# Performance work log

Measured on AMD Instinct MI355X. Metric: run time of the kernel, lower is better.

## Reference

```python
import jax, jax.numpy as jnp
import numpy as np

DN = ('NHWC', 'HWIO', 'NHWC')
EPS = 1e-3  # Keras BatchNormalization default epsilon


def conv2d(x, w):
    return jax.lax.conv_general_dilated(x, w, (1, 1), 'SAME', dimension_numbers=DN)


def hard_sigmoid(x):
    # Keras ConvLSTM2D default recurrent_activation
    return jnp.clip(0.2 * x + 0.5, 0.0, 1.0)


def convlstm2d(x, Wx, Wh, b):
    """Keras ConvLSTM2D, return_sequences=True. x: (B,T,H,W,C).
    Wx: (3,3,C,4F) input kernel, Wh: (3,3,F,4F) recurrent kernel, b: (4F,).
    Gate order (Keras): i, f, c, o."""
    B, T, H, W, C = x.shape
    F = Wh.shape[2]
    # input-to-gate convs for all timesteps in one batched conv
    xg = conv2d(x.reshape(B * T, H, W, C), Wx) + b          # (B*T,H,W,4F)
    xg = xg.reshape(B, T, H, W, 4 * F).transpose(1, 0, 2, 3, 4)  # (T,B,H,W,4F)

    def step(carry, xg_t):
        h, c = carry
        g = xg_t + conv2d(h, Wh)                            # (B,H,W,4F)
        i, f, cc, o = jnp.split(g, 4, axis=-1)
        i = hard_sigmoid(i)
        f = hard_sigmoid(f)
        o = hard_sigmoid(o)
        c = f * c + i * jnp.tanh(cc)
        h = o * jnp.tanh(c)
        return (h, c), h

    h0 = jnp.zeros((B, H, W, F), x.dtype)
    (_, _), hs = jax.lax.scan(step, (h0, h0), xg)           # hs: (T,B,H,W,F)
    return hs.transpose(1, 0, 2, 3, 4)


def batchnorm(x, gamma, beta):
    # training-mode BN over all axes except channel (last)
    mu = x.mean(axis=(0, 1, 2, 3), keepdims=True)
    var = x.var(axis=(0, 1, 2, 3), keepdims=True)
    return gamma * (x - mu) * jax.lax.rsqrt(var + EPS) + beta


def setup_inputs() -> dict:
    key = jax.random.key(0)
    B, T, H, W, C = 4, 8, 16, 16, 256
    F = 256
    ks = jax.random.split(key, 10)
    s = 0.02
    inp = {
        'input_tensor': jax.random.normal(ks[0], (B, T, H, W, C), jnp.float32),
        'Wx1': jax.random.normal(ks[1], (3, 3, C, 4 * F), jnp.float32) * s,
        'Wh1': jax.random.normal(ks[2], (3, 3, F, 4 * F), jnp.float32) * s,
        'b1': jnp.zeros((4 * F,), jnp.float32),
        'g1': jnp.ones((F,), jnp.float32),
        'be1': jnp.zeros((F,), jnp.float32),
        'Wx2': jax.random.normal(ks[3], (3, 3, F, 4 * F), jnp.float32) * s,
        'Wh2': jax.random.normal(ks[4], (3, 3, F, 4 * F), jnp.float32) * s,
        'b2': jnp.zeros((4 * F,), jnp.float32),
        'g2': jnp.ones((F,), jnp.float32),
        'be2': jnp.zeros((F,), jnp.float32),
        'Wx3': jax.random.normal(ks[5], (3, 3, F, 4 * F), jnp.float32) * s,
        'Wh3': jax.random.normal(ks[6], (3, 3, F, 4 * F), jnp.float32) * s,
        'b3': jnp.zeros((4 * F,), jnp.float32),
        'g3': jnp.ones((F,), jnp.float32),
        'be3': jnp.zeros((F,), jnp.float32),
    }
    return inp


def reference(input_tensor, Wx1, Wh1, b1, g1, be1,
              Wx2, Wh2, b2, g2, be2,
              Wx3, Wh3, b3, g3, be3):
    x = batchnorm(convlstm2d(input_tensor, Wx1, Wh1, b1), g1, be1)
    x = batchnorm(convlstm2d(x, Wx2, Wh2, b2), g2, be2)
    x = batchnorm(convlstm2d(x, Wx3, Wh3, b3), g3, be3)
    return x
```

## Files before the change

### kernel.cpp

```cpp
#include <hip/hip_runtime.h>

#define HW      256
#define COUT    1024
#define TSTEPS  8
#define BN_EPS  1e-3f
#define KTOT    2304

typedef unsigned short u16;
typedef unsigned int   u32;
typedef __attribute__((ext_vector_type(8))) _Float16 v8h;
typedef __attribute__((ext_vector_type(4))) float v4f;

__device__ __forceinline__ u16 f2h(float x) {
    _Float16 h = (_Float16)x; return *(u16*)&h;
}
__device__ __forceinline__ float h2f(u16 u) {
    _Float16 h = *(_Float16*)&u; return (float)h;
}
__device__ __forceinline__ float hsig(float x) {
    return fminf(fmaxf(0.2f * x + 0.5f, 0.f), 1.f);
}

typedef __attribute__((address_space(1))) const unsigned int gas_u32;
typedef __attribute__((address_space(3))) unsigned int las_u32;
__device__ __forceinline__ void gl16(const void* g, void* l) {
    __builtin_amdgcn_global_load_lds((gas_u32*)g, (las_u32*)l, 16, 0, 0);
}

__global__ __launch_bounds__(256, 2) void conv_big_k(
    const u16* __restrict__ apad,
    const u16* __restrict__ wT,
    const float* __restrict__ bias,
    u16* __restrict__ out)
{
    constexpr int KQ = 36;
    __shared__ u16 lds[2 * 16384];

    const int bid = blockIdx.x;
    const int xcd = bid & 7, idx = bid >> 3;
    const int by = (xcd >> 1) * 2 + (idx & 1);
    const int bx = (xcd & 1) * 32 + (idx >> 1);
    const int m0 = bx * 128, n0 = by * 128;
    const int tid = threadIdx.x, lane = tid & 63, w = tid >> 6;
    const int wr = w >> 1, wc = w & 1;
    const int lr = lane >> 3;
    const int g  = (lane & 7) ^ lr;
    const int fr = lane & 15, kc = lane >> 4;

    const char* a_src[4];
    #pragma unroll
    for (int i = 0; i < 4; ++i) {
        int m = m0 + w * 32 + i * 8 + lr;
        int img = m >> 8, pix = m & 255, yy = pix >> 4, xx = pix & 15;
        a_src[i] = (const char*)apad + ((((long)img * 18 + yy) * 18 + xx) * 256 + g * 8) * 2;
    }
    const char* b_src[4];
    #pragma unroll
    for (int i = 0; i < 4; ++i) {
        int n = n0 + w * 32 + i * 8 + lr;
        b_src[i] = (const char*)wT + ((long)n * KTOT + g * 8) * 2;
    }

    int aro[4][2], bro[4][2];
    #pragma unroll
    for (int mi = 0; mi < 4; ++mi) {
        int rl = wr * 64 + mi * 16 + fr;
        #pragma unroll
        for (int ks = 0; ks < 2; ++ks)
            aro[mi][ks] = rl * 128 + ((((ks << 2) | kc) ^ (fr & 7)) << 4);
    }
    #pragma unroll
    for (int ni = 0; ni < 4; ++ni) {
        int nr = wc * 64 + ni * 16 + fr;
        #pragma unroll
        for (int ks = 0; ks < 2; ++ks)
            bro[ni][ks] = 16384 + nr * 128 + ((((ks << 2) | kc) ^ (fr & 7)) << 4);
    }

    v4f acc[4][4];
    #pragma unroll
    for (int mi = 0; mi < 4; ++mi)
        #pragma unroll
        for (int ni = 0; ni < 4; ++ni) acc[mi][ni] = (v4f)0.f;

#define STAGE_B(J) { int j_ = (J); int dxy = j_ >> 2, c64 = j_ & 3;           \
    int dy = (dxy * 11) >> 5; int dx = dxy - dy * 3;                          \
    int aoff = ((dy * 18 + dx) * 256 + c64 * 64) * 2; int boff = j_ * 128;    \
    char* base = (char*)lds + (j_ & 1) * 32768;                               \
    _Pragma("unroll") for (int i = 0; i < 4; ++i)                             \
        gl16(a_src[i] + aoff, base + (w * 32 + i * 8) * 128);                 \
    _Pragma("unroll") for (int i = 0; i < 4; ++i)                             \
        gl16(b_src[i] + boff, base + 16384 + (w * 32 + i * 8) * 128); }

#define COMPUTE_B(J) { const char* base = (const char*)lds + ((J) & 1) * 32768; \
    v8h af[4][2], bf[4][2];                                                   \
    _Pragma("unroll") for (int mi = 0; mi < 4; ++mi)                          \
        _Pragma("unroll") for (int ks = 0; ks < 2; ++ks)                      \
            af[mi][ks] = *(const v8h*)(base + aro[mi][ks]);                   \
    _Pragma("unroll") for (int ni = 0; ni < 4; ++ni)                          \
        _Pragma("unroll") for (int ks = 0; ks < 2; ++ks)                      \
            bf[ni][ks] = *(const v8h*)(base + bro[ni][ks]);                   \
    __builtin_amdgcn_s_setprio(1);                                            \
    _Pragma("unroll") for (int ks = 0; ks < 2; ++ks)                          \
    _Pragma("unroll") for (int mi = 0; mi < 4; ++mi)                          \
    _Pragma("unroll") for (int ni = 0; ni < 4; ++ni)                          \
        acc[mi][ni] = __builtin_amdgcn_mfma_f32_16x16x32_f16(af[mi][ks], bf[ni][ks], acc[mi][ni], 0, 0, 0); \
    __builtin_amdgcn_s_setprio(0); }

    STAGE_B(0);
    for (int kq = 0; kq < KQ; ++kq) {
        int jj = kq + 1 < KQ ? kq + 1 : KQ - 1;
        __builtin_amdgcn_s_barrier();
        STAGE_B(jj);
        asm volatile("s_waitcnt vmcnt(8)" ::: "memory");
        __builtin_amdgcn_s_barrier();
        __builtin_amdgcn_sched_barrier(0);
        COMPUTE_B(kq);
    }
#undef STAGE_B
#undef COMPUTE_B

    #pragma unroll
    for (int mi = 0; mi < 4; ++mi) {
        #pragma unroll
        for (int ni = 0; ni < 4; ++ni) {
            int mrow = m0 + wr * 64 + mi * 16 + ((lane >> 4) << 2);
            int ncol = n0 + wc * 64 + ni * 16 + fr;
            float b0 = bias[(ncol & 3) * 256 + (ncol >> 2)];
            #pragma unroll
            for (int r = 0; r < 4; ++r)
                out[(long)(mrow + r) * COUT + ncol] = f2h(acc[mi][ni][r] + b0);
        }
    }
}

__global__ __launch_bounds__(256, 2) void rec_fused_k(
    const u16* __restrict__ ph_in,
    const u16* __restrict__ wTf,
    const u16* __restrict__ xg,
    float* __restrict__ cbuf,
    float* __restrict__ hs,
    u16* __restrict__ ph_out,
    int t)
{
    __shared__ u16 lds[3 * 2048];

    const int bid = blockIdx.x;
    const int by = (bid & 7) * 2 + ((bid >> 3) & 1);
    const int bx = bid >> 4;
    const int m0 = bx * 32, n0 = by * 64;
    const int tid = threadIdx.x, lane = tid & 63, w = tid >> 6;
    const int wr = w >> 1, wc = w & 1;
    const int fr = lane & 15, kc = lane >> 4;

    const char* a_src;
    {
        int rt = tid >> 3;
        int gg = (lane & 7) ^ (rt & 7);
        int m = m0 + rt;
        int img = m >> 8, pix = m & 255, yy = pix >> 4, xx = pix & 15;
        a_src = (const char*)ph_in + ((((long)img * 18 + yy) * 18 + xx) * 256 + gg * 8) * 2;
    }
    const char* b_base0 = (const char*)wTf + ((long)(by * 4 + wc * 2 + 0) * 72) * 1024 + lane * 16;
    const char* b_base1 = (const char*)wTf + ((long)(by * 4 + wc * 2 + 1) * 72) * 1024 + lane * 16;

    int aro[2];
    #pragma unroll
    for (int ks = 0; ks < 2; ++ks)
        aro[ks] = (wr * 16 + fr) * 128 + ((((ks << 2) | kc) ^ (fr & 7)) << 4);

    v4f acc0 = (v4f)0.f, acc1 = (v4f)0.f;

#define STAGE_A(J) { int j_ = (J); int dxy = j_ >> 2, c64 = j_ & 3;           \
    int dy = (dxy * 11) >> 5; int dx = dxy - dy * 3;                          \
    int aoff = ((dy * 18 + dx) * 256 + c64 * 64) * 2;                         \
    gl16(a_src + aoff, (char*)lds + (j_ % 3) * 4096 + w * 1024); }

#define LDB(J, R00, R01, R10, R11) {                                          \
    R00 = *(const v8h*)(b_base0 + (2 * (J)) * 1024);                          \
    R01 = *(const v8h*)(b_base0 + (2 * (J) + 1) * 1024);                      \
    R10 = *(const v8h*)(b_base1 + (2 * (J)) * 1024);                          \
    R11 = *(const v8h*)(b_base1 + (2 * (J) + 1) * 1024); }

#define BODY(KQ, C00, C01, C10, C11, L00, L01, L10, L11) {                    \
    int kq_ = (KQ); int jj_ = kq_ + 2 < 36 ? kq_ + 2 : 35;                    \
    asm volatile("s_waitcnt vmcnt(5)" ::: "memory");                          \
    __builtin_amdgcn_s_barrier();                                             \
    __builtin_amdgcn_sched_barrier(0);                                        \
    LDB(jj_, L00, L01, L10, L11);                                             \
    STAGE_A(jj_);                                                             \
    const char* base_ = (const char*)lds + (kq_ % 3) * 4096;                  \
    v8h af0_ = *(const v8h*)(base_ + aro[0]);                                 \
    v8h af1_ = *(const v8h*)(base_ + aro[1]);                                 \
    __builtin_amdgcn_s_setprio(1);                                            \
    acc0 = __builtin_amdgcn_mfma_f32_16x16x32_f16(af0_, C00, acc0, 0, 0, 0);  \
    acc1 = __builtin_amdgcn_mfma_f32_16x16x32_f16(af0_, C10, acc1, 0, 0, 0);  \
    acc0 = __builtin_amdgcn_mfma_f32_16x16x32_f16(af1_, C01, acc0, 0, 0, 0);  \
    acc1 = __builtin_amdgcn_mfma_f32_16x16x32_f16(af1_, C11, acc1, 0, 0, 0);  \
    __builtin_amdgcn_s_setprio(0); }

    v8h A00, A01, A10, A11, B00, B01, B10, B11, C00, C01, C10, C11;
    LDB(0, A00, A01, A10, A11); STAGE_A(0);
    LDB(1, B00, B01, B10, B11); STAGE_A(1);
    for (int j = 0; j < 12; ++j) {
        int k0 = 3 * j;
        BODY(k0,     A00, A01, A10, A11, C00, C01, C10, C11);
        BODY(k0 + 1, B00, B01, B10, B11, A00, A01, A10, A11);
        BODY(k0 + 2, C00, C01, C10, C11, B00, B01, B10, B11);
    }
#undef STAGE_A
#undef LDB
#undef BODY

    v4f accA[2] = {acc0, acc1};
    const bool gl0 = lane & 1, gl1 = lane & 2;
    #pragma unroll
    for (int ni = 0; ni < 2; ++ni) {
        float V0 = accA[ni][0], V1 = accA[ni][1];
        float V2 = accA[ni][2], V3 = accA[ni][3];
        float x0 = __shfl_xor(V0, 1), x1 = __shfl_xor(V1, 1);
        float x2 = __shfl_xor(V2, 1), x3 = __shfl_xor(V3, 1);
        float a0 = gl0 ? x1 : V0;
        float a1 = gl0 ? V1 : x0;
        float a2 = gl0 ? x3 : V2;
        float a3 = gl0 ? V3 : x2;
        float s0 = __shfl_xor(a0, 2), s1 = __shfl_xor(a1, 2);
        float s2 = __shfl_xor(a2, 2), s3 = __shfl_xor(a3, 2);
        float Ti = gl1 ? s2 : a0;
        float Tf = gl1 ? s3 : a1;
        float Tc = gl1 ? a2 : s0;
        float To = gl1 ? a3 : s1;

        int row = m0 + wr * 16 + ((lane >> 4) << 2) + (lane & 3);
        int f4  = n0 + wc * 32 + ni * 16 + (lane & 12);
        int img = row >> 8, pix = row & 255, fch = f4 >> 2;
        long xrow = ((long)(img * TSTEPS + t) * HW + pix);
        uint2 xb = *(const uint2*)&xg[xrow * COUT + f4];
        float pi = Ti + h2f((u16)(xb.x & 0xffff));
        float pf = Tf + h2f((u16)(xb.x >> 16));
        float pc = Tc + h2f((u16)(xb.y & 0xffff));
        float po = To + h2f((u16)(xb.y >> 16));
        long cidx = (long)row * 256 + fch;
        float c = hsig(pf) * cbuf[cidx] + hsig(pi) * tanhf(pc);
        float h = hsig(po) * tanhf(c);
        cbuf[cidx] = c;
        hs[xrow * 256 + fch] = h;
        int yy = pix >> 4, xx = pix & 15;
        ph_out[(((long)img * 18 + yy + 1) * 18 + xx + 1) * 256 + fch] = f2h(h);
    }
}

__global__ __launch_bounds__(256) void gates0_k(
    const u16* __restrict__ xg, float* __restrict__ cbuf,
    float* __restrict__ hs, u16* __restrict__ ph_out)
{
    int idx = blockIdx.x * 256 + threadIdx.x;
    int fch = idx & 255, row = idx >> 8;
    int img = row >> 8, pix = row & 255;
    long xrow = (long)(img * TSTEPS) * HW + pix;
    uint2 xb = *(const uint2*)&xg[xrow * COUT + fch * 4];
    float pi = h2f((u16)(xb.x & 0xffff));
    float pc = h2f((u16)(xb.y & 0xffff));
    float po = h2f((u16)(xb.y >> 16));
    float c = hsig(pi) * tanhf(pc);
    float h = hsig(po) * tanhf(c);
    cbuf[(long)row * 256 + fch] = c;
    hs[xrow * 256 + fch] = h;
    int yy = pix >> 4, xx = pix & 15;
    ph_out[(((long)img * 18 + yy + 1) * 18 + xx + 1) * 256 + fch] = f2h(h);
}

__global__ __launch_bounds__(256) void wprep_k(const float* __restrict__ w,
                                               u16* __restrict__ wT)
{
    int k0 = blockIdx.x * 32;
    int np = blockIdx.y * 256 + threadIdx.x;
    int n  = (np & 3) * 256 + (np >> 2);
    u32 pk[16];
    #pragma unroll
    for (int kk = 0; kk < 32; kk += 2) {
        float a = w[(long)(k0 + kk) * COUT + n];
        float b = w[(long)(k0 + kk + 1) * COUT + n];
        pk[kk >> 1] = (u32)f2h(a) | ((u32)f2h(b) << 16);
    }
    uint4* dst = (uint4*)&wT[(long)np * KTOT + k0];
    dst[0] = make_uint4(pk[0], pk[1], pk[2], pk[3]);
    dst[1] = make_uint4(pk[4], pk[5], pk[6], pk[7]);
    dst[2] = make_uint4(pk[8], pk[9], pk[10], pk[11]);
    dst[3] = make_uint4(pk[12], pk[13], pk[14], pk[15]);
}

__global__ __launch_bounds__(256) void wprep_frag_k(const float* __restrict__ w,
                                                    u16* __restrict__ wTf)
{
    int kq = blockIdx.x;
    int nf = blockIdx.y * 4 + (threadIdx.x >> 6);
    int l  = threadIdx.x & 63;
    int np = nf * 16 + (l & 15);
    int n  = (np & 3) * 256 + (np >> 2);
    int k0 = kq * 32 + (l >> 4) * 8;
    u32 pk[4];
    #pragma unroll
    for (int e = 0; e < 8; e += 2) {
        float a = w[(long)(k0 + e) * COUT + n];
        float b = w[(long)(k0 + e + 1) * COUT + n];
        pk[e >> 1] = (u32)f2h(a) | ((u32)f2h(b) << 16);
    }
    *(uint4*)&wTf[((long)(nf * 72) + kq) * 512 + l * 8] =
        make_uint4(pk[0], pk[1], pk[2], pk[3]);
}

__global__ __launch_bounds__(256) void convert_x_k(const float* __restrict__ x,
                                                   u16* __restrict__ padx)
{
    int q = blockIdx.x * 256 + threadIdx.x;
    int e0 = q * 4;
    int f = e0 & 255, pix = (e0 >> 8) & 255, img = e0 >> 16;
    float4 v = ((const float4*)x)[q];
    int yy = pix >> 4, xx = pix & 15;
    long o = (((long)img * 18 + yy + 1) * 18 + xx + 1) * 256 + f;
    u32 lo = (u32)f2h(v.x) | ((u32)f2h(v.y) << 16);
    u32 hi = (u32)f2h(v.z) | ((u32)f2h(v.w) << 16);
    *(uint2*)&padx[o] = make_uint2(lo, hi);
}

__global__ __launch_bounds__(256) void bn_stats1_k(
    const float* __restrict__ x, float* __restrict__ partial)
{
    const int tid = threadIdx.x;
    const int blk = blockIdx.x;
    float s = 0.f, s2 = 0.f;
    const long base = (long)blk * 128 * 256;
    #pragma unroll 8
    for (int gi = 0; gi < 128; ++gi) {
        float v = x[base + gi * 256 + tid];
        s += v; s2 += v * v;
    }
    partial[blk * 512 + tid]       = s;
    partial[blk * 512 + 256 + tid] = s2;
}

__global__ __launch_bounds__(256) void bn_stats2_k(
    const float* __restrict__ partial, const float* __restrict__ gamma,
    const float* __restrict__ beta, float* __restrict__ stats)
{
    const int f = threadIdx.x;
    float s = 0.f, s2 = 0.f;
    #pragma unroll 8
    for (int b = 0; b < 64; ++b) {
        s  += partial[b * 512 + f];
        s2 += partial[b * 512 + 256 + f];
    }
    const float inv_n = 1.f / 8192.f;
    float mu  = s * inv_n;
    float var = s2 * inv_n - mu * mu;
    float sc  = gamma[f] * rsqrtf(var + BN_EPS);
    stats[f]       = sc;
    stats[256 + f] = beta[f] - mu * sc;
}

__global__ __launch_bounds__(256) void bn_apply_k(
    const float* __restrict__ x, const float* __restrict__ stats,
    u16* __restrict__ padx, float* __restrict__ out)
{
    const int q = blockIdx.x * 256 + threadIdx.x;
    const int e0 = q * 4;
    const int f = e0 & 255, pix = (e0 >> 8) & 255, img = e0 >> 16;
    float4 v  = ((const float4*)x)[q];
    float4 sc = *(const float4*)(stats + f);
    float4 sh = *(const float4*)(stats + 256 + f);
    v.x = v.x * sc.x + sh.x;
    v.y = v.y * sc.y + sh.y;
    v.z = v.z * sc.z + sh.z;
    v.w = v.w * sc.w + sh.w;
    if (out) ((float4*)out)[q] = v;
    if (padx) {
        int yy = pix >> 4, xx = pix & 15;
        long o = (((long)img * 18 + yy + 1) * 18 + xx + 1) * 256 + f;
        u32 lo = (u32)f2h(v.x) | ((u32)f2h(v.y) << 16);
        u32 hi = (u32)f2h(v.z) | ((u32)f2h(v.w) << 16);
        *(uint2*)&padx[o] = make_uint2(lo, hi);
    }
}

extern "C" void kernel_launch(void* const* d_in, const int* in_sizes, int n_in,
                              void* d_out, int out_size, void* d_ws, size_t ws_size,
                              hipStream_t stream)
{
    const float* x0    = (const float*)d_in[0];
    const float* Wx[3] = {(const float*)d_in[1], (const float*)d_in[6],  (const float*)d_in[11]};
    const float* Wh[3] = {(const float*)d_in[2], (const float*)d_in[7],  (const float*)d_in[12]};
    const float* bb[3] = {(const float*)d_in[3], (const float*)d_in[8],  (const float*)d_in[13]};
    const float* gg[3] = {(const float*)d_in[4], (const float*)d_in[9],  (const float*)d_in[14]};
    const float* be[3] = {(const float*)d_in[5], (const float*)d_in[10], (const float*)d_in[15]};

    float* ws    = (float*)d_ws;
    u16*  xg     = (u16*)ws;
    float* cbuf  = ws   + 4194304;
    float* hs    = cbuf + 262144;
    float* part  = hs   + 2097152;
    float* stats = part + 262144;
    u16*  pad_x  = (u16*)(stats + 512);
    u16*  pad_h  = pad_x + 2654208;
    u16*  wTx    = pad_h + 663552;
    u16*  wTf    = wTx   + 2359296;
    const long PHN = 331776;

    hipMemsetAsync(pad_x, 0, 2654208 * sizeof(u16), stream);
    hipMemsetAsync(pad_h, 0, 2 * PHN * sizeof(u16), stream);
    hipLaunchKernelGGL(convert_x_k, dim3(2048), dim3(256), 0, stream, x0, pad_x);

    for (int l = 0; l < 3; ++l) {
        hipLaunchKernelGGL(wprep_k, dim3(72, 4), dim3(256), 0, stream, Wx[l], wTx);
        hipLaunchKernelGGL(wprep_frag_k, dim3(72, 16), dim3(256), 0, stream, Wh[l], wTf);

        hipLaunchKernelGGL(conv_big_k, dim3(512), dim3(256), 0, stream,
            pad_x, wTx, bb[l], xg);

        hipLaunchKernelGGL(gates0_k, dim3(1024), dim3(256), 0, stream,
            xg, cbuf, hs, pad_h + PHN);

        for (int t = 1; t < TSTEPS; ++t) {
            hipLaunchKernelGGL(rec_fused_k, dim3(512), dim3(256), 0, stream,
                pad_h + (t & 1) * PHN, wTf, xg, cbuf, hs,
                pad_h + ((t & 1) ^ 1) * PHN, t);
        }

        hipLaunchKernelGGL(bn_stats1_k, dim3(64), dim3(256), 0, stream, hs, part);
        hipLaunchKernelGGL(bn_stats2_k, dim3(1), dim3(256), 0, stream, part, gg[l], be[l], stats);
        hipLaunchKernelGGL(bn_apply_k, dim3(2048), dim3(256), 0, stream, hs, stats,
            (l < 2) ? pad_x : (u16*)nullptr, (l == 2) ? (float*)d_out : (float*)nullptr);
    }
}
```

Baseline: 541.8 us.

## Enlarge recurrent kernel tile to 64x64 with 8 waves; simplify conv_big pipeline

The recurrent fused gate kernel now uses 512-thread blocks covering 64 rows by 64 gate columns, so each wave holds one B column fragment and two A row fragments. This halves the grid and the per-wave B register loads, raising reuse of the weight fragments. The conv_big loop is also changed to wait for all loads before issuing the next stage, which removes the partial vmcnt overlap and adds a peeled final iteration. Fewer blocks (256) may underfill the GPU's CUs, and the stricter wait may expose load latency in the input convolution.

```diff
diff --git a/kernel.cpp b/kernel.cpp
--- a/kernel.cpp
+++ b/kernel.cpp
@@ -108,15 +108,17 @@
     __builtin_amdgcn_s_setprio(0); }
 
     STAGE_B(0);
-    for (int kq = 0; kq < KQ; ++kq) {
-        int jj = kq + 1 < KQ ? kq + 1 : KQ - 1;
-        __builtin_amdgcn_s_barrier();
-        STAGE_B(jj);
-        asm volatile("s_waitcnt vmcnt(8)" ::: "memory");
+    for (int kq = 0; kq < KQ - 1; ++kq) {
+        asm volatile("s_waitcnt vmcnt(0)" ::: "memory");
         __builtin_amdgcn_s_barrier();
         __builtin_amdgcn_sched_barrier(0);
+        STAGE_B(kq + 1);
         COMPUTE_B(kq);
     }
+    asm volatile("s_waitcnt vmcnt(0)" ::: "memory");
+    __builtin_amdgcn_s_barrier();
+    __builtin_amdgcn_sched_barrier(0);
+    COMPUTE_B(KQ - 1);
 #undef STAGE_B
 #undef COMPUTE_B
 
@@ -134,7 +136,7 @@
     }
 }
 
-__global__ __launch_bounds__(256, 2) void rec_fused_k(
+__global__ __launch_bounds__(512) void rec_fused_k(
     const u16* __restrict__ ph_in,
     const u16* __restrict__ wTf,
     const u16* __restrict__ xg,
@@ -143,70 +145,70 @@
     u16* __restrict__ ph_out,
     int t)
 {
-    __shared__ u16 lds[3 * 2048];
+    __shared__ u16 lds[3 * 4096];
 
     const int bid = blockIdx.x;
     const int by = (bid & 7) * 2 + ((bid >> 3) & 1);
     const int bx = bid >> 4;
-    const int m0 = bx * 32, n0 = by * 64;
+    const int m0 = bx * 64, n0 = by * 64;
     const int tid = threadIdx.x, lane = tid & 63, w = tid >> 6;
-    const int wr = w >> 1, wc = w & 1;
+    const int wr = w >> 2, wc = w & 3;
     const int fr = lane & 15, kc = lane >> 4;
 
     const char* a_src;
     {
         int rt = tid >> 3;
-        int gg = (lane & 7) ^ (rt & 7);
+        int gg = (tid & 7) ^ (rt & 7);
         int m = m0 + rt;
         int img = m >> 8, pix = m & 255, yy = pix >> 4, xx = pix & 15;
         a_src = (const char*)ph_in + ((((long)img * 18 + yy) * 18 + xx) * 256 + gg * 8) * 2;
     }
-    const char* b_base0 = (const char*)wTf + ((long)(by * 4 + wc * 2 + 0) * 72) * 1024 + lane * 16;
-    const char* b_base1 = (const char*)wTf + ((long)(by * 4 + wc * 2 + 1) * 72) * 1024 + lane * 16;
-
-    int aro[2];
-    #pragma unroll
-    for (int ks = 0; ks < 2; ++ks)
-        aro[ks] = (wr * 16 + fr) * 128 + ((((ks << 2) | kc) ^ (fr & 7)) << 4);
+    const char* b_base = (const char*)wTf + ((long)(by * 4 + wc) * 72) * 1024 + lane * 16;
+
+    int aro[2][2];
+    #pragma unroll
+    for (int mi = 0; mi < 2; ++mi)
+        #pragma unroll
+        for (int ks = 0; ks < 2; ++ks)
+            aro[mi][ks] = (wr * 32 + mi * 16 + fr) * 128 + ((((ks << 2) | kc) ^ (fr & 7)) << 4);
 
     v4f acc0 = (v4f)0.f, acc1 = (v4f)0.f;
 
 #define STAGE_A(J) { int j_ = (J); int dxy = j_ >> 2, c64 = j_ & 3;           \
     int dy = (dxy * 11) >> 5; int dx = dxy - dy * 3;                          \
     int aoff = ((dy * 18 + dx) * 256 + c64 * 64) * 2;                         \
-    gl16(a_src + aoff, (char*)lds + (j_ % 3) * 4096 + w * 1024); }
-
-#define LDB(J, R00, R01, R10, R11) {                                          \
-    R00 = *(const v8h*)(b_base0 + (2 * (J)) * 1024);                          \
-    R01 = *(const v8h*)(b_base0 + (2 * (J) + 1) * 1024);                      \
-    R10 = *(const v8h*)(b_base1 + (2 * (J)) * 1024);                          \
-    R11 = *(const v8h*)(b_base1 + (2 * (J) + 1) * 1024); }
-
-#define BODY(KQ, C00, C01, C10, C11, L00, L01, L10, L11) {                    \
+    gl16(a_src + aoff, (char*)lds + (j_ % 3) * 8192 + w * 1024); }
+
+#define LDB(J, R0, R1) { R0 = *(const v8h*)(b_base + (2 * (J)) * 1024);       \
+                         R1 = *(const v8h*)(b_base + (2 * (J) + 1) * 1024); }
+
+#define BODY(KQ, C0, C1, L0, L1) {                                            \
     int kq_ = (KQ); int jj_ = kq_ + 2 < 36 ? kq_ + 2 : 35;                    \
-    asm volatile("s_waitcnt vmcnt(5)" ::: "memory");                          \
+    asm volatile("s_waitcnt vmcnt(3)" ::: "memory");                          \
     __builtin_amdgcn_s_barrier();                                             \
     __builtin_amdgcn_sched_barrier(0);                                        \
-    LDB(jj_, L00, L01, L10, L11);                                             \
+    LDB(jj_, L0, L1);                                                         \
     STAGE_A(jj_);                                                             \
-    const char* base_ = (const char*)lds + (kq_ % 3) * 4096;                  \
-    v8h af0_ = *(const v8h*)(base_ + aro[0]);                                 \
-    v8h af1_ = *(const v8h*)(base_ + aro[1]);                                 \
+    const char* base_ = (const char*)lds + (kq_ % 3) * 8192;                  \
+    v8h af00_ = *(const v8h*)(base_ + aro[0][0]);                             \
+    v8h af10_ = *(const v8h*)(base_ + aro[1][0]);                             \
+    v8h af01_ = *(const v8h*)(base_ + aro[0][1]);                             \
+    v8h af11_ = *(const v8h*)(base_ + aro[1][1]);                             \
     __builtin_amdgcn_s_setprio(1);                                            \
-    acc0 = __builtin_amdgcn_mfma_f32_16x16x32_f16(af0_, C00, acc0, 0, 0, 0);  \
-    acc1 = __builtin_amdgcn_mfma_f32_16x16x32_f16(af0_, C10, acc1, 0, 0, 0);  \
-    acc0 = __builtin_amdgcn_mfma_f32_16x16x32_f16(af1_, C01, acc0, 0, 0, 0);  \
-    acc1 = __builtin_amdgcn_mfma_f32_16x16x32_f16(af1_, C11, acc1, 0, 0, 0);  \
+    acc0 = __builtin_amdgcn_mfma_f32_16x16x32_f16(af00_, C0, acc0, 0, 0, 0);  \
+    acc1 = __builtin_amdgcn_mfma_f32_16x16x32_f16(af10_, C0, acc1, 0, 0, 0);  \
+    acc0 = __builtin_amdgcn_mfma_f32_16x16x32_f16(af01_, C1, acc0, 0, 0, 0);  \
+    acc1 = __builtin_amdgcn_mfma_f32_16x16x32_f16(af11_, C1, acc1, 0, 0, 0);  \
     __builtin_amdgcn_s_setprio(0); }
 
-    v8h A00, A01, A10, A11, B00, B01, B10, B11, C00, C01, C10, C11;
-    LDB(0, A00, A01, A10, A11); STAGE_A(0);
-    LDB(1, B00, B01, B10, B11); STAGE_A(1);
+    v8h A0, A1, B0, B1, C0, C1;
+    LDB(0, A0, A1); STAGE_A(0);
+    LDB(1, B0, B1); STAGE_A(1);
     for (int j = 0; j < 12; ++j) {
         int k0 = 3 * j;
-        BODY(k0,     A00, A01, A10, A11, C00, C01, C10, C11);
-        BODY(k0 + 1, B00, B01, B10, B11, A00, A01, A10, A11);
-        BODY(k0 + 2, C00, C01, C10, C11, B00, B01, B10, B11);
+        BODY(k0,     A0, A1, C0, C1);
+        BODY(k0 + 1, B0, B1, A0, A1);
+        BODY(k0 + 2, C0, C1, B0, B1);
     }
 #undef STAGE_A
 #undef LDB
@@ -215,9 +217,9 @@
     v4f accA[2] = {acc0, acc1};
     const bool gl0 = lane & 1, gl1 = lane & 2;
     #pragma unroll
-    for (int ni = 0; ni < 2; ++ni) {
-        float V0 = accA[ni][0], V1 = accA[ni][1];
-        float V2 = accA[ni][2], V3 = accA[ni][3];
+    for (int mi = 0; mi < 2; ++mi) {
+        float V0 = accA[mi][0], V1 = accA[mi][1];
+        float V2 = accA[mi][2], V3 = accA[mi][3];
         float x0 = __shfl_xor(V0, 1), x1 = __shfl_xor(V1, 1);
         float x2 = __shfl_xor(V2, 1), x3 = __shfl_xor(V3, 1);
         float a0 = gl0 ? x1 : V0;
@@ -231,8 +233,8 @@
         float Tc = gl1 ? a2 : s0;
         float To = gl1 ? a3 : s1;
 
-        int row = m0 + wr * 16 + ((lane >> 4) << 2) + (lane & 3);
-        int f4  = n0 + wc * 32 + ni * 16 + (lane & 12);
+        int row = m0 + wr * 32 + mi * 16 + ((lane >> 4) << 2) + (lane & 3);
+        int f4  = n0 + wc * 16 + (lane & 12);
         int img = row >> 8, pix = row & 255, fch = f4 >> 2;
         long xrow = ((long)(img * TSTEPS + t) * HW + pix);
         uint2 xb = *(const uint2*)&xg[xrow * COUT + f4];
@@ -421,7 +423,7 @@
             xg, cbuf, hs, pad_h + PHN);
 
         for (int t = 1; t < TSTEPS; ++t) {
-            hipLaunchKernelGGL(rec_fused_k, dim3(512), dim3(256), 0, stream,
+            hipLaunchKernelGGL(rec_fused_k, dim3(256), dim3(512), 0, stream,
                 pad_h + (t & 1) * PHN, wTf, xg, cbuf, hs,
                 pad_h + ((t & 1) ^ 1) * PHN, t);
         }
```

Measured after the change: 504.2 us. -6.9%, faster.
